# Optimization experiments

Measured on AMD Instinct MI355X. Metric: run time of the kernel, lower is better.

The kernel has to match this reference:

```python
import jax, jax.numpy as jnp
import numpy as np

N, S, I, F, M = 1024, 8, 128, 1024, 512


def setup_inputs() -> dict:
    key = jax.random.key(0)
    ks = jax.random.split(key, 16)
    sc_x = 0.02  # weight init scale (gain details don't change the op structure)
    d = {
        "modulation": jax.random.normal(ks[0], (N, S * I), dtype=jnp.float32),
        # per-gate grouped weights: input-proj [S, F, I], hidden-proj [S, F, F], bias [S, F]
        "Wxi": jax.random.normal(ks[1], (S, F, I), dtype=jnp.float32) * sc_x,
        "Whi": jax.random.normal(ks[2], (S, F, F), dtype=jnp.float32) * sc_x,
        "bi": jnp.full((S, F), -1.0, dtype=jnp.float32),  # init_input
        "Wxf": jax.random.normal(ks[3], (S, F, I), dtype=jnp.float32) * sc_x,
        "Whf": jax.random.normal(ks[4], (S, F, F), dtype=jnp.float32) * sc_x,
        "bf": jnp.full((S, F), 1.0, dtype=jnp.float32),  # init_forget
        "Wxg": jax.random.normal(ks[5], (S, F, I), dtype=jnp.float32) * sc_x,
        "Whg": jax.random.normal(ks[6], (S, F, F), dtype=jnp.float32) * sc_x,
        "bg": jnp.zeros((S, F), dtype=jnp.float32),
        "Wxo": jax.random.normal(ks[7], (S, F, I), dtype=jnp.float32) * sc_x,
        "Who": jax.random.normal(ks[8], (S, F, F), dtype=jnp.float32) * sc_x,
        "bo": jnp.zeros((S, F), dtype=jnp.float32),
        # out projection [S, M, F] + bias
        "Wout": jax.random.normal(ks[9], (S, M, F), dtype=jnp.float32) * sc_x,
        "bout": jnp.zeros((S, M), dtype=jnp.float32),
    }
    return d


def reference(modulation, Wxi, Whi, bi, Wxf, Whf, bf, Wxg, Whg, bg, Wxo, Who, bo, Wout, bout):
    x = modulation.reshape(N, S, I)  # grouped per-stream input
    # first call: no past state -> h = c = zeros([1, S*F]) (broadcasts over N)
    h0 = jnp.zeros((1, S, F), dtype=modulation.dtype)
    c0 = jnp.zeros((1, S, F), dtype=modulation.dtype)

    def gate(Wx, Wh, b):
        # Accumulate([Linear(x), Linear(h)]): block-diagonal (grouped) matmuls
        return (jnp.einsum('nsi,sfi->nsf', x, Wx)
                + jnp.einsum('msf,sgf->msg', h0, Wh)
                + b)

    i = jax.nn.sigmoid(gate(Wxi, Whi, bi))
    f = jax.nn.sigmoid(gate(Wxf, Whf, bf))
    g = jnp.tanh(gate(Wxg, Whg, bg))
    o = jax.nn.sigmoid(gate(Wxo, Who, bo))
    c = f * c0 + i * g            # [N, S, F]
    h = o * jnp.tanh(c)           # [N, S, F]  (dropout p=0 -> identity)
    out = jnp.einsum('nsf,smf->nsm', h, Wout) + bout  # [N, S, M]
    return out.reshape(N, S * M)
```

## Files before the change

kernel.cpp:

```cpp
#include <hip/hip_runtime.h>

#define N_ 1024
#define S_ 8
#define I_ 128
#define F_ 1024
#define M_ 512

typedef unsigned short ushort_t;
typedef __attribute__((ext_vector_type(8))) short bf16x8;
typedef __attribute__((ext_vector_type(4))) float f32x4;

__device__ __forceinline__ unsigned short f2bf(float x) {
    unsigned int u = __float_as_uint(x);
    u += 0x7fffu + ((u >> 16) & 1u);
    return (unsigned short)(u >> 16);
}

__device__ __forceinline__ float sigmoidf_(float x) {
    return 1.f / (1.f + __expf(-x));
}
__device__ __forceinline__ float tanhf_(float x) {
    float xc = fminf(fmaxf(x, -15.f), 15.f);
    float e = __expf(2.f * xc);
    return (e - 1.f) / (e + 1.f);
}

__device__ __forceinline__ void gload_lds16(const ushort_t* g, ushort_t* l) {
    __builtin_amdgcn_global_load_lds((const __attribute__((address_space(1))) void*)g,
                                     (__attribute__((address_space(3))) void*)l, 16, 0, 0);
}

__global__ __launch_bounds__(256) void k_convert(
    const float* __restrict__ mod, const float* __restrict__ wxi,
    const float* __restrict__ wxg, const float* __restrict__ wxo,
    const float* __restrict__ wout, ushort_t* __restrict__ ws) {
    unsigned v = blockIdx.x * 256u + threadIdx.x;
    const float4* src; unsigned idx; ushort_t* dst;
    if (v < 262144u)       { src = (const float4*)mod;  idx = v;            dst = ws; }
    else if (v < 524288u)  { src = (const float4*)wxi;  idx = v - 262144u;  dst = ws + 1048576; }
    else if (v < 786432u)  { src = (const float4*)wxg;  idx = v - 524288u;  dst = ws + 2097152; }
    else if (v < 1048576u) { src = (const float4*)wxo;  idx = v - 786432u;  dst = ws + 3145728; }
    else                   { src = (const float4*)wout; idx = v - 1048576u; dst = ws + 4194304; }
    float4 f = src[idx];
    ushort4 o;
    o.x = f2bf(f.x); o.y = f2bf(f.y); o.z = f2bf(f.z); o.w = f2bf(f.w);
    ((ushort4*)dst)[idx] = o;
}

__global__ __launch_bounds__(256, 2) void k_gates(
    const ushort_t* __restrict__ xb, const ushort_t* __restrict__ wib,
    const ushort_t* __restrict__ wgb, const ushort_t* __restrict__ wob,
    const float* __restrict__ bi, const float* __restrict__ bg,
    const float* __restrict__ bo, ushort_t* __restrict__ hb) {
    const int Lb   = blockIdx.x + 16 * blockIdx.y + 128 * blockIdx.z;
    const int s    = Lb & 7;
    const int slot = Lb >> 3;
    const int n0   = (slot & 7) * 128;
    const int f0   = (slot >> 3) * 64;
    __shared__ ushort_t sA[128 * 72];
    __shared__ ushort_t sB[3][64 * 72];
    const int tid  = threadIdx.x;
    const int lane = tid & 63;
    const int cl   = lane & 15;
    const int quad = lane >> 4;
    const int w    = tid >> 6;
    const int wm   = (w >> 1) * 64;
    const int wn   = (w & 1) * 32;

    f32x4 acc[3][4][2];
    #pragma unroll
    for (int g = 0; g < 3; ++g)
        #pragma unroll
        for (int mt = 0; mt < 4; ++mt)
            #pragma unroll
            for (int nt = 0; nt < 2; ++nt)
                acc[g][mt][nt] = (f32x4){0.f, 0.f, 0.f, 0.f};

    const ushort_t* wb0 = wib + (size_t)s * (F_ * I_);
    const ushort_t* wb1 = wgb + (size_t)s * (F_ * I_);
    const ushort_t* wb2 = wob + (size_t)s * (F_ * I_);

    for (int k0 = 0; k0 < 128; k0 += 64) {
        #pragma unroll
        for (int i = 0; i < 5; ++i) {
            unsigned c = (unsigned)tid + i * 256u;
            if (c < 1152u) {
                unsigned row = c / 9u, kc = c % 9u;
                unsigned kce = kc < 8u ? kc : 7u;
                gload_lds16(xb + (size_t)(n0 + row) * (S_ * I_) + s * I_ + k0 + kce * 8,
                            sA + c * 8);
            }
        }
        #pragma unroll
        for (int i = 0; i < 3; ++i) {
            unsigned c = (unsigned)tid + i * 256u;
            if (c < 576u) {
                unsigned row = c / 9u, kc = c % 9u;
                unsigned kce = kc < 8u ? kc : 7u;
                size_t goff = (size_t)(f0 + row) * I_ + k0 + kce * 8;
                gload_lds16(wb0 + goff, &sB[0][c * 8]);
                gload_lds16(wb1 + goff, &sB[1][c * 8]);
                gload_lds16(wb2 + goff, &sB[2][c * 8]);
            }
        }
        __syncthreads();
        #pragma unroll
        for (int kk = 0; kk < 2; ++kk) {
            const int kb = kk * 32 + quad * 8;
            bf16x8 a[4];
            #pragma unroll
            for (int mt = 0; mt < 4; ++mt)
                a[mt] = *(const bf16x8*)(sA + (wm + mt * 16 + cl) * 72 + kb);
            #pragma unroll
            for (int g = 0; g < 3; ++g) {
                #pragma unroll
                for (int nt = 0; nt < 2; ++nt) {
                    bf16x8 b = *(const bf16x8*)(&sB[g][(wn + nt * 16 + cl) * 72 + kb]);
                    #pragma unroll
                    for (int mt = 0; mt < 4; ++mt)
                        acc[g][mt][nt] = __builtin_amdgcn_mfma_f32_16x16x32_bf16(
                            a[mt], b, acc[g][mt][nt], 0, 0, 0);
                }
            }
        }
        __syncthreads();
    }

    #pragma unroll
    for (int nt = 0; nt < 2; ++nt) {
        int fc = f0 + wn + nt * 16 + cl;
        float bii = bi[s * F_ + fc], bgg = bg[s * F_ + fc], boo = bo[s * F_ + fc];
        #pragma unroll
        for (int mt = 0; mt < 4; ++mt) {
            #pragma unroll
            for (int r = 0; r < 4; ++r) {
                int nr = n0 + wm + mt * 16 + quad * 4 + r;
                float pi = acc[0][mt][nt][r] + bii;
                float pg = acc[1][mt][nt][r] + bgg;
                float po = acc[2][mt][nt][r] + boo;
                float hv = sigmoidf_(po) * tanhf_(sigmoidf_(pi) * tanhf_(pg));
                hb[(size_t)s * (N_ * F_) + (size_t)nr * F_ + fc] = f2bf(hv);
            }
        }
    }
}

__global__ __launch_bounds__(256, 2) void k_out(
    const ushort_t* __restrict__ hb, const ushort_t* __restrict__ woutb,
    const float* __restrict__ bout, float* __restrict__ out) {
    const int Lb   = blockIdx.x + 8 * blockIdx.y + 64 * blockIdx.z;
    const int s    = Lb & 7;
    const int slot = Lb >> 3;
    const int n0   = (slot & 7) * 128;
    const int m0   = (slot >> 3) * 64;
    __shared__ ushort_t sA[128 * 136];
    __shared__ ushort_t sB[64 * 136];
    const int tid  = threadIdx.x;
    const int lane = tid & 63;
    const int cl   = lane & 15;
    const int quad = lane >> 4;
    const int w    = tid >> 6;
    const int wm   = (w >> 1) * 64;
    const int wn   = (w & 1) * 32;

    f32x4 acc[4][2];
    #pragma unroll
    for (int mt = 0; mt < 4; ++mt)
        #pragma unroll
        for (int nt = 0; nt < 2; ++nt)
            acc[mt][nt] = (f32x4){0.f, 0.f, 0.f, 0.f};

    const ushort_t* ha = hb + (size_t)s * (N_ * F_);
    const ushort_t* wa = woutb + (size_t)s * (M_ * F_);

    for (int k0 = 0; k0 < 1024; k0 += 128) {
        #pragma unroll
        for (int i = 0; i < 9; ++i) {
            unsigned c = (unsigned)tid + i * 256u;
            if (c < 2176u) {
                unsigned row = c / 17u, kc = c % 17u;
                unsigned kce = kc < 16u ? kc : 15u;
                gload_lds16(ha + (size_t)(n0 + row) * F_ + k0 + kce * 8, sA + c * 8);
            }
        }
        #pragma unroll
        for (int i = 0; i < 5; ++i) {
            unsigned c = (unsigned)tid + i * 256u;
            if (c < 1088u) {
                unsigned row = c / 17u, kc = c % 17u;
                unsigned kce = kc < 16u ? kc : 15u;
                gload_lds16(wa + (size_t)(m0 + row) * F_ + k0 + kce * 8, sB + c * 8);
            }
        }
        __syncthreads();
        #pragma unroll
        for (int kk = 0; kk < 4; ++kk) {
            const int kb = kk * 32 + quad * 8;
            bf16x8 a[4], b[2];
            #pragma unroll
            for (int mt = 0; mt < 4; ++mt)
                a[mt] = *(const bf16x8*)(sA + (wm + mt * 16 + cl) * 136 + kb);
            #pragma unroll
            for (int nt = 0; nt < 2; ++nt)
                b[nt] = *(const bf16x8*)(sB + (wn + nt * 16 + cl) * 136 + kb);
            #pragma unroll
            for (int nt = 0; nt < 2; ++nt)
                #pragma unroll
                for (int mt = 0; mt < 4; ++mt)
                    acc[mt][nt] = __builtin_amdgcn_mfma_f32_16x16x32_bf16(
                        a[mt], b[nt], acc[mt][nt], 0, 0, 0);
        }
        __syncthreads();
    }

    #pragma unroll
    for (int nt = 0; nt < 2; ++nt) {
        int mc = m0 + wn + nt * 16 + cl;
        float bb = bout[s * M_ + mc];
        #pragma unroll
        for (int mt = 0; mt < 4; ++mt) {
            #pragma unroll
            for (int r = 0; r < 4; ++r) {
                int nr = n0 + wm + mt * 16 + quad * 4 + r;
                out[(size_t)nr * (S_ * M_) + s * M_ + mc] = acc[mt][nt][r] + bb;
            }
        }
    }
}

extern "C" void kernel_launch(void* const* d_in, const int* in_sizes, int n_in,
                              void* d_out, int out_size, void* d_ws, size_t ws_size,
                              hipStream_t stream) {
    const float* mod  = (const float*)d_in[0];
    const float* Wxi  = (const float*)d_in[1];
    const float* bi   = (const float*)d_in[3];
    const float* Wxg  = (const float*)d_in[7];
    const float* bg   = (const float*)d_in[9];
    const float* Wxo  = (const float*)d_in[10];
    const float* bo   = (const float*)d_in[12];
    const float* Wout = (const float*)d_in[13];
    const float* bout = (const float*)d_in[14];

    ushort_t* ws  = (ushort_t*)d_ws;
    ushort_t* xb  = ws;
    ushort_t* wib = ws + 1048576;
    ushort_t* wgb = ws + 2097152;
    ushort_t* wob = ws + 3145728;
    ushort_t* wtb = ws + 4194304;
    ushort_t* hb  = ws + 8388608;

    k_convert<<<8192, 256, 0, stream>>>(mod, Wxi, Wxg, Wxo, Wout, ws);
    k_gates<<<dim3(16, 8, 8), 256, 0, stream>>>(xb, wib, wgb, wob, bi, bg, bo, hb);
    k_out<<<dim3(8, 8, 8), 256, 0, stream>>>(hb, wtb, bout, (float*)d_out);
}
```

Before: 211.8 us.

## Fuse fp32-to-bf16 conversion into GEMM tile loads and drop convert kernel

Removes the separate conversion kernel and instead loads fp32 inputs and weights directly inside the gate and output GEMM kernels, converting to bf16 in registers before storing into shared memory. This avoids a full write and re-read of bf16 copies of x, the three gate weight sets and Wout, plus one kernel launch. In exchange the tile loads become synchronous register round-trips instead of async global-to-LDS loads. Each fp32 weight tile is also fetched by several blocks, so more bytes are read per tile than with bf16 copies.

```diff
diff --git a/kernel.cpp b/kernel.cpp
--- a/kernel.cpp
+++ b/kernel.cpp
@@ -8,6 +8,7 @@
 
 typedef unsigned short ushort_t;
 typedef __attribute__((ext_vector_type(8))) short bf16x8;
+typedef __attribute__((ext_vector_type(8))) unsigned short u16x8;
 typedef __attribute__((ext_vector_type(4))) float f32x4;
 
 __device__ __forceinline__ unsigned short f2bf(float x) {
@@ -30,26 +31,18 @@
                                      (__attribute__((address_space(3))) void*)l, 16, 0, 0);
 }
 
-__global__ __launch_bounds__(256) void k_convert(
-    const float* __restrict__ mod, const float* __restrict__ wxi,
+__device__ __forceinline__ void cvt_store8(const float* __restrict__ gp, ushort_t* lp) {
+    float4 a = ((const float4*)gp)[0];
+    float4 b = ((const float4*)gp)[1];
+    u16x8 v;
+    v[0] = f2bf(a.x); v[1] = f2bf(a.y); v[2] = f2bf(a.z); v[3] = f2bf(a.w);
+    v[4] = f2bf(b.x); v[5] = f2bf(b.y); v[6] = f2bf(b.z); v[7] = f2bf(b.w);
+    *(u16x8*)lp = v;
+}
+
+__global__ __launch_bounds__(256, 2) void k_gates(
+    const float* __restrict__ x, const float* __restrict__ wxi,
     const float* __restrict__ wxg, const float* __restrict__ wxo,
-    const float* __restrict__ wout, ushort_t* __restrict__ ws) {
-    unsigned v = blockIdx.x * 256u + threadIdx.x;
-    const float4* src; unsigned idx; ushort_t* dst;
-    if (v < 262144u)       { src = (const float4*)mod;  idx = v;            dst = ws; }
-    else if (v < 524288u)  { src = (const float4*)wxi;  idx = v - 262144u;  dst = ws + 1048576; }
-    else if (v < 786432u)  { src = (const float4*)wxg;  idx = v - 524288u;  dst = ws + 2097152; }
-    else if (v < 1048576u) { src = (const float4*)wxo;  idx = v - 786432u;  dst = ws + 3145728; }
-    else                   { src = (const float4*)wout; idx = v - 1048576u; dst = ws + 4194304; }
-    float4 f = src[idx];
-    ushort4 o;
-    o.x = f2bf(f.x); o.y = f2bf(f.y); o.z = f2bf(f.z); o.w = f2bf(f.w);
-    ((ushort4*)dst)[idx] = o;
-}
-
-__global__ __launch_bounds__(256, 2) void k_gates(
-    const ushort_t* __restrict__ xb, const ushort_t* __restrict__ wib,
-    const ushort_t* __restrict__ wgb, const ushort_t* __restrict__ wob,
     const float* __restrict__ bi, const float* __restrict__ bg,
     const float* __restrict__ bo, ushort_t* __restrict__ hb) {
     const int Lb   = blockIdx.x + 16 * blockIdx.y + 128 * blockIdx.z;
@@ -76,32 +69,27 @@
             for (int nt = 0; nt < 2; ++nt)
                 acc[g][mt][nt] = (f32x4){0.f, 0.f, 0.f, 0.f};
 
-    const ushort_t* wb0 = wib + (size_t)s * (F_ * I_);
-    const ushort_t* wb1 = wgb + (size_t)s * (F_ * I_);
-    const ushort_t* wb2 = wob + (size_t)s * (F_ * I_);
+    const float* wb0 = wxi + (size_t)s * (F_ * I_);
+    const float* wb1 = wxg + (size_t)s * (F_ * I_);
+    const float* wb2 = wxo + (size_t)s * (F_ * I_);
 
     for (int k0 = 0; k0 < 128; k0 += 64) {
         #pragma unroll
-        for (int i = 0; i < 5; ++i) {
-            unsigned c = (unsigned)tid + i * 256u;
-            if (c < 1152u) {
-                unsigned row = c / 9u, kc = c % 9u;
-                unsigned kce = kc < 8u ? kc : 7u;
-                gload_lds16(xb + (size_t)(n0 + row) * (S_ * I_) + s * I_ + k0 + kce * 8,
-                            sA + c * 8);
-            }
-        }
-        #pragma unroll
-        for (int i = 0; i < 3; ++i) {
-            unsigned c = (unsigned)tid + i * 256u;
-            if (c < 576u) {
-                unsigned row = c / 9u, kc = c % 9u;
-                unsigned kce = kc < 8u ? kc : 7u;
-                size_t goff = (size_t)(f0 + row) * I_ + k0 + kce * 8;
-                gload_lds16(wb0 + goff, &sB[0][c * 8]);
-                gload_lds16(wb1 + goff, &sB[1][c * 8]);
-                gload_lds16(wb2 + goff, &sB[2][c * 8]);
-            }
+        for (int i = 0; i < 4; ++i) {
+            int c = tid + i * 256;
+            int row = c >> 3, kc = c & 7;
+            cvt_store8(x + (size_t)(n0 + row) * (S_ * I_) + s * I_ + k0 + kc * 8,
+                       sA + row * 72 + kc * 8);
+        }
+        #pragma unroll
+        for (int i = 0; i < 2; ++i) {
+            int c = tid + i * 256;
+            int row = c >> 3, kc = c & 7;
+            size_t goff = (size_t)(f0 + row) * I_ + k0 + kc * 8;
+            ushort_t* loff0 = &sB[0][row * 72 + kc * 8];
+            cvt_store8(wb0 + goff, loff0);
+            cvt_store8(wb1 + goff, &sB[1][row * 72 + kc * 8]);
+            cvt_store8(wb2 + goff, &sB[2][row * 72 + kc * 8]);
         }
         __syncthreads();
         #pragma unroll
@@ -146,7 +134,7 @@
 }
 
 __global__ __launch_bounds__(256, 2) void k_out(
-    const ushort_t* __restrict__ hb, const ushort_t* __restrict__ woutb,
+    const ushort_t* __restrict__ hb, const float* __restrict__ wout,
     const float* __restrict__ bout, float* __restrict__ out) {
     const int Lb   = blockIdx.x + 8 * blockIdx.y + 64 * blockIdx.z;
     const int s    = Lb & 7;
@@ -171,7 +159,7 @@
             acc[mt][nt] = (f32x4){0.f, 0.f, 0.f, 0.f};
 
     const ushort_t* ha = hb + (size_t)s * (N_ * F_);
-    const ushort_t* wa = woutb + (size_t)s * (M_ * F_);
+    const float*    wa = wout + (size_t)s * (M_ * F_);
 
     for (int k0 = 0; k0 < 1024; k0 += 128) {
         #pragma unroll
@@ -184,13 +172,11 @@
             }
         }
         #pragma unroll
-        for (int i = 0; i < 5; ++i) {
-            unsigned c = (unsigned)tid + i * 256u;
-            if (c < 1088u) {
-                unsigned row = c / 17u, kc = c % 17u;
-                unsigned kce = kc < 16u ? kc : 15u;
-                gload_lds16(wa + (size_t)(m0 + row) * F_ + k0 + kce * 8, sB + c * 8);
-            }
+        for (int i = 0; i < 4; ++i) {
+            int c = tid + i * 256;
+            int row = c >> 4, kc = c & 15;
+            cvt_store8(wa + (size_t)(m0 + row) * F_ + k0 + kc * 8,
+                       sB + row * 136 + kc * 8);
         }
         __syncthreads();
         #pragma unroll
@@ -241,15 +227,8 @@
     const float* Wout = (const float*)d_in[13];
     const float* bout = (const float*)d_in[14];
 
-    ushort_t* ws  = (ushort_t*)d_ws;
-    ushort_t* xb  = ws;
-    ushort_t* wib = ws + 1048576;
-    ushort_t* wgb = ws + 2097152;
-    ushort_t* wob = ws + 3145728;
-    ushort_t* wtb = ws + 4194304;
-    ushort_t* hb  = ws + 8388608;
-
-    k_convert<<<8192, 256, 0, stream>>>(mod, Wxi, Wxg, Wxo, Wout, ws);
-    k_gates<<<dim3(16, 8, 8), 256, 0, stream>>>(xb, wib, wgb, wob, bi, bg, bo, hb);
-    k_out<<<dim3(8, 8, 8), 256, 0, stream>>>(hb, wtb, bout, (float*)d_out);
-}
+    ushort_t* hb = (ushort_t*)d_ws;
+
+    k_gates<<<dim3(16, 8, 8), 256, 0, stream>>>(mod, Wxi, Wxg, Wxo, bi, bg, bo, hb);
+    k_out<<<dim3(8, 8, 8), 256, 0, stream>>>(hb, Wout, bout, (float*)d_out);
+}
```

Result: slower. 216.8 us (+2.4%).
